# Performance work log

Hardware: AMD Instinct MI355X
Metric: run time of the kernel (lower is better)

Reference implementation:

```python
import jax, jax.numpy as jnp
import numpy as np

WS = 8  # window/grid size, hard-coded in GlobalCirculationBlock
NH = 8  # num_heads


def _ln(x, w, b):
    m = jnp.mean(x, -1, keepdims=True)
    v = jnp.mean((x - m) ** 2, -1, keepdims=True)
    return (x - m) * jax.lax.rsqrt(v + 1e-5) * w + b


def _attn(q, k, v, scale):
    # q,k,v: [..., S, hd]
    s = jnp.einsum('...qd,...kd->...qk', q, k) * scale
    return jnp.einsum('...qk,...kd->...qd', jax.nn.softmax(s, axis=-1), v)


def setup_inputs() -> dict:
    key = jax.random.key(0)
    ks = jax.random.split(key, 8)
    B, C, H, W = 8, 128, 128, 128
    hid = 4 * C
    f = lambda k, shape, s=0.02: jax.random.normal(k, shape, jnp.float32) * s
    z = lambda n: jnp.zeros((n,), jnp.float32)
    return {
        'x': f(ks[0], (B, C, H, W), 1.0),
        'conv_w': f(ks[1], (C, 1, 3, 3)),        # depthwise 3x3 pos embed
        'conv_b': z(C),
        'norm1_w': jnp.ones((C,), jnp.float32), 'norm1_b': z(C),
        'wqkv': f(ks[2], (C, 3 * C)),            # qkv_bias=False
        'proj_w': f(ks[3], (C, C)), 'proj_b': z(C),
        'norm2_w': jnp.ones((C,), jnp.float32), 'norm2_b': z(C),
        'fc1_w': f(ks[4], (C, hid)), 'fc1_b': z(hid),
        'fc2_w': f(ks[5], (hid, C)), 'fc2_b': z(C),
        'ls1': jnp.full((C,), 1e-2, jnp.float32),
        'ls2': jnp.full((C,), 1e-2, jnp.float32),
    }


def reference(x, conv_w, conv_b, norm1_w, norm1_b, wqkv, proj_w, proj_b,
              norm2_w, norm2_b, fc1_w, fc1_b, fc2_w, fc2_b, ls1, ls2):
    B, C, H, W = x.shape
    nh, ws = NH, WS
    hd = C // nh
    scale = hd ** -0.5
    nhl = nh // 2                     # local heads == global heads
    nH, nW = H // ws, W // ws         # H,W multiples of ws -> no padding

    # depthwise conv positional embedding + residual
    pos = jax.lax.conv_general_dilated(
        x, conv_w, (1, 1), 'SAME',
        dimension_numbers=('NCHW', 'OIHW', 'NCHW'), feature_group_count=C)
    x = x + pos + conv_b[None, :, None, None]

    xt = x.reshape(B, C, H * W).transpose(0, 2, 1)   # [B, N, C]

    # ---- dual-scale attention ----
    xn = _ln(xt, norm1_w, norm1_b).reshape(B, H, W, C)
    qkv = (xn @ wqkv).reshape(B, H, W, 3, nh, hd)
    q, k, v = qkv[:, :, :, 0], qkv[:, :, :, 1], qkv[:, :, :, 2]  # [B,H,W,nh,hd]

    # local branch: first nhl heads, window attention (seq = ws*ws)
    def win(t):  # [B,H,W,nhl,hd] -> [B,nH,nW,nhl,ws*ws,hd]
        t = t.reshape(B, nH, ws, nW, ws, nhl, hd)
        return t.transpose(0, 1, 3, 5, 2, 4, 6).reshape(B, nH, nW, nhl, ws * ws, hd)

    ol = _attn(win(q[..., :nhl, :]), win(k[..., :nhl, :]), win(v[..., :nhl, :]), scale)
    ol = (ol.reshape(B, nH, nW, nhl, ws, ws, hd)
            .transpose(0, 1, 4, 2, 5, 3, 6)
            .reshape(B, H, W, nhl * hd))

    # global branch: last nhl heads, grid attention (seq = nH*nW)
    def grd(t):  # [B,H,W,nhl,hd] -> [B,ws,ws,nhl,nH*nW,hd]
        t = t.reshape(B, nH, ws, nW, ws, nhl, hd)
        return t.transpose(0, 2, 4, 5, 1, 3, 6).reshape(B, ws, ws, nhl, nH * nW, hd)

    og = _attn(grd(q[..., nhl:, :]), grd(k[..., nhl:, :]), grd(v[..., nhl:, :]), scale)
    og = (og.reshape(B, ws, ws, nhl, nH, nW, hd)
            .transpose(0, 4, 1, 5, 2, 3, 6)
            .reshape(B, H, W, nhl * hd))

    a = jnp.concatenate([ol, og], axis=-1).reshape(B, H * W, C)
    a = a @ proj_w + proj_b
    xt = xt + ls1 * a

    # ---- MLP ----
    h = _ln(xt, norm2_w, norm2_b)
    h = jax.nn.gelu(h @ fc1_w + fc1_b, approximate=False) @ fc2_w + fc2_b
    xt = xt + ls2 * h

    return xt.transpose(0, 2, 1).reshape(B, C, H, W)
```

## Files before the change

kernel.cpp:

```cpp
#include <hip/hip_runtime.h>
#include <hip/hip_bf16.h>

typedef __hip_bfloat16 bf16;
typedef __attribute__((ext_vector_type(8))) short short8;
typedef __attribute__((ext_vector_type(4))) short short4v;
typedef __attribute__((ext_vector_type(4))) float floatx4;
typedef __attribute__((ext_vector_type(16))) float floatx16;

#define Bn 8
#define Cc 128
#define Hh 128
#define Wl 128
#define HW (Hh*Wl)
#define NT (Bn*HW)
#define REG 8388608

#define QSCALE 0.36067376022224085f
#if __has_builtin(__builtin_amdgcn_exp2f)
#define EXP2(x) __builtin_amdgcn_exp2f(x)
#else
#define EXP2(x) __expf((x)*0.69314718055994531f)
#endif

__device__ __forceinline__ float b2f(bf16 v){ return __bfloat162float(v); }
__device__ __forceinline__ bf16  f2b(float v){ return __float2bfloat16(v); }

#define GL16(gp, lp) __builtin_amdgcn_global_load_lds( \
    (__attribute__((address_space(1))) unsigned int*)(gp), \
    (__attribute__((address_space(3))) unsigned int*)(lp), 16, 0, 0)

__global__ __launch_bounds__(256) void transpose_all(const float* __restrict__ wqkv,
                                                     const float* __restrict__ proj_w,
                                                     const float* __restrict__ fc1_w,
                                                     const float* __restrict__ fc2_w,
                                                     bf16* __restrict__ qkvT,
                                                     bf16* __restrict__ projT,
                                                     bf16* __restrict__ fc1T,
                                                     bf16* __restrict__ fc2T){
  int idx = blockIdx.x*256 + threadIdx.x;
  const float* src; bf16* dst; int K, N;
  if(idx < 49152){ src=wqkv; dst=qkvT; K=128; N=384; }
  else if(idx < 65536){ idx -= 49152; src=proj_w; dst=projT; K=128; N=128; }
  else if(idx < 131072){ idx -= 65536; src=fc1_w; dst=fc1T; K=128; N=512; }
  else { idx -= 131072; src=fc2_w; dst=fc2T; K=512; N=128; }
  int n = idx % N, k = idx / N;
  dst[(size_t)n*K + k] = f2b(src[idx]);
}

__global__ __launch_bounds__(256) void conv_kernel(const float* __restrict__ x,
                                                   const float* __restrict__ cw,
                                                   const float* __restrict__ cb,
                                                   float* __restrict__ xt){
  __shared__ float tile[16][132];
  int blk = blockIdx.x;
  int h = blk & 127; int t = blk >> 7;
  int cg = t & 7;    int b = t >> 3;
  int w4 = threadIdx.x & 31;
  int ci = threadIdx.x >> 5;
  int w0 = w4*4;
#pragma unroll
  for(int cc=0; cc<2; cc++){
    int c = cg*16 + ci*2 + cc;
    const float* xp = x + ((size_t)(b*Cc + c))*HW;
    float wg[9];
#pragma unroll
    for(int i=0;i<9;i++) wg[i] = cw[c*9+i];
    float4 rowv[3]; float lf[3], rt[3];
#pragma unroll
    for(int r=0;r<3;r++){
      int hh = h-1+r;
      float4 v = {0.f,0.f,0.f,0.f};
      if(hh>=0 && hh<Hh) v = *(const float4*)(xp + hh*Wl + w0);
      rowv[r] = v;
      float l = __shfl_up(v.w, 1, 32);
      float rr = __shfl_down(v.x, 1, 32);
      lf[r] = (w4==0)  ? 0.f : l;
      rt[r] = (w4==31) ? 0.f : rr;
    }
    float acc0 = cb[c], acc1 = cb[c], acc2 = cb[c], acc3 = cb[c];
#pragma unroll
    for(int r=0;r<3;r++){
      float4 v = rowv[r];
      acc0 += wg[r*3+0]*lf[r] + wg[r*3+1]*v.x + wg[r*3+2]*v.y;
      acc1 += wg[r*3+0]*v.x   + wg[r*3+1]*v.y + wg[r*3+2]*v.z;
      acc2 += wg[r*3+0]*v.y   + wg[r*3+1]*v.z + wg[r*3+2]*v.w;
      acc3 += wg[r*3+0]*v.z   + wg[r*3+1]*v.w + wg[r*3+2]*rt[r];
    }
    acc0 += rowv[1].x; acc1 += rowv[1].y; acc2 += rowv[1].z; acc3 += rowv[1].w;
    float4 o = {acc0, acc1, acc2, acc3};
    *(float4*)&tile[ci*2+cc][w0] = o;
  }
  __syncthreads();
  const size_t obase = ((size_t)b*HW + (size_t)h*Wl)*Cc + cg*16;
#pragma unroll
  for(int i=0;i<8;i++){
    int idx = i*256 + threadIdx.x;
    int c2 = idx & 15, w2 = idx >> 4;
    xt[obase + (size_t)w2*Cc + c2] = tile[c2][w2];
  }
}

__global__ __launch_bounds__(256) void ln_kernel(const float* __restrict__ xt,
                                                 const float* __restrict__ wv,
                                                 const float* __restrict__ bv,
                                                 bf16* __restrict__ xn){
  int tok  = blockIdx.x*4 + (threadIdx.x>>6);
  int lane = threadIdx.x & 63;
  const float* row = xt + (size_t)tok*Cc;
  float v0 = row[lane], v1 = row[lane+64];
  float s = v0+v1;
#pragma unroll
  for(int off=32; off; off>>=1) s += __shfl_down(s, off, 64);
  s = __shfl(s, 0, 64);
  float m = s * (1.0f/128.0f);
  float d0 = v0-m, d1 = v1-m;
  float vs = d0*d0 + d1*d1;
#pragma unroll
  for(int off=32; off; off>>=1) vs += __shfl_down(vs, off, 64);
  vs = __shfl(vs, 0, 64);
  float rstd = rsqrtf(vs*(1.0f/128.0f) + 1e-5f);
  bf16* orow = xn + (size_t)tok*Cc;
  orow[lane]    = f2b(d0*rstd*wv[lane]    + bv[lane]);
  orow[lane+64] = f2b(d1*rstd*wv[lane+64] + bv[lane+64]);
}

template<int EPI>
__global__ __launch_bounds__(256) void mfma_gemm(const bf16* __restrict__ A,
                                                 const bf16* __restrict__ Wt,
                                                 const float* __restrict__ bias,
                                                 bf16* __restrict__ outb,
                                                 float* __restrict__ xt,
                                                 const float* __restrict__ ls,
                                                 int N, int K){
  __shared__ short As[2][128*32];
  __shared__ short Bs[2][64*32];
  const int tid  = threadIdx.x;
  const int lane = tid & 63;
  const int w    = tid >> 6;

  const int nwg = gridDim.x * gridDim.y;
  const int lin = blockIdx.y * gridDim.x + blockIdx.x;
  const int t   = (lin & 7) * (nwg >> 3) + (lin >> 3);
  const int m0  = (t / gridDim.x) * 128;
  const int n0  = (t % gridDim.x) * 64;

  const int l1 = tid + 256;
  const bf16* gA0 = A  + (size_t)(m0 + ((tid>>6)<<4) + (tid&15))*K + (((tid>>4)&3)<<3);
  const bf16* gA1 = A  + (size_t)(m0 + ((l1 >>6)<<4) + (l1 &15))*K + (((l1 >>4)&3)<<3);
  const bf16* gB  = Wt + (size_t)(n0 + ((tid>>6)<<4) + (tid&15))*K + (((tid>>4)&3)<<3);
  const int ldsA0 = w*512;
  const int ldsA1 = 2048 + w*512;
  const int ldsB  = w*512;

  floatx4 acc[4][2];
#pragma unroll
  for(int i=0;i<4;i++)
#pragma unroll
    for(int j=0;j<2;j++) acc[i][j] = (floatx4){0.f,0.f,0.f,0.f};

  const int nk = K >> 5;
  GL16(gA0, &As[0][ldsA0]);
  GL16(gA1, &As[0][ldsA1]);
  GL16(gB , &Bs[0][ldsB ]);
  __syncthreads();

  int cur = 0;
  for(int it=0; it<nk; ++it){
    if(it+1 < nk){
      const int kn = (it+1) << 5;
      GL16(gA0 + kn, &As[cur^1][ldsA0]);
      GL16(gA1 + kn, &As[cur^1][ldsA1]);
      GL16(gB  + kn, &Bs[cur^1][ldsB ]);
    }
    short8 af[4], bfr[2];
#pragma unroll
    for(int mt=0;mt<4;mt++) af[mt] = *(short8*)&As[cur][(((w&1)*4+mt)*64 + lane)*8];
#pragma unroll
    for(int nt=0;nt<2;nt++) bfr[nt] = *(short8*)&Bs[cur][(((w>>1)*2+nt)*64 + lane)*8];
#pragma unroll
    for(int mt=0;mt<4;mt++)
#pragma unroll
      for(int nt=0;nt<2;nt++)
        acc[mt][nt] = __builtin_amdgcn_mfma_f32_16x16x32_bf16(af[mt], bfr[nt], acc[mt][nt], 0, 0, 0);
    __syncthreads();
    cur ^= 1;
  }

#pragma unroll
  for(int mt=0;mt<4;mt++){
#pragma unroll
    for(int nt=0;nt<2;nt++){
#pragma unroll
      for(int r=0;r<4;r++){
        int row = m0 + (w&1)*64 + mt*16 + ((lane>>4))*4 + r;
        int col = n0 + (w>>1)*32 + nt*16 + (lane&15);
        float v = acc[mt][nt][r];
        if(EPI==0){
          int reg = col >> 6;
          int head = (col >> 4) & 3;
          int ch = col & 15;
          int b = row >> 14, h = (row >> 7) & 127, ww = row & 127;
          if(reg < 2) v *= QSCALE;
          size_t didx;
          if(!(reg & 1)){
            int inst = ((b*16 + (h>>3))*16 + (ww>>3))*4 + head;
            int pos = (h&7)*8 + (ww&7);
            didx = ((size_t)inst*64 + pos)*16 + ch;
          } else {
            int inst = ((b*8 + (h&7))*8 + (ww&7))*4 + head;
            int pos = (h>>3)*16 + (ww>>3);
            didx = ((size_t)inst*256 + pos)*16 + ch;
          }
          outb[(size_t)reg*REG + didx] = f2b(v);
        } else if(EPI==2){
          v += bias[col];
          xt[(size_t)row*128 + col] += ls[col]*v;
        }
      }
    }
  }
}

__global__ __launch_bounds__(256) void fused_mlp(const bf16* A,
                                                 const bf16* __restrict__ W1,
                                                 const float* __restrict__ b1,
                                                 const bf16* __restrict__ W2,
                                                 const float* __restrict__ b2,
                                                 const float* __restrict__ xt,
                                                 const float* __restrict__ ls,
                                                 bf16* outb){
  extern __shared__ short lds[];
  const int W1OFF = 0, W2OFF = 8192, HSOFF = 16384;
  const int tid = threadIdx.x, lane = tid & 63, w = tid >> 6;
  const int n16 = lane & 15, quad = lane >> 4;
  const int lin = blockIdx.x;
  const int t = (lin & 7)*128 + (lin >> 3);
  const int mw = t*128 + w*32;

  auto stage = [&](int nc, int buf){
    const bf16* W1c = W1 + (size_t)nc*32*128;
#pragma unroll
    for(int p=0;p<2;p++){
      int fid = p*4 + w;
      int nt = fid >> 2, ks = fid & 3;
      GL16(W1c + (size_t)(nt*16 + n16)*128 + ks*32 + quad*8, &lds[W1OFF + buf*4096 + fid*512]);
      GL16(W2 + (size_t)(fid*16 + n16)*512 + nc*32 + quad*8, &lds[W2OFF + buf*4096 + fid*512]);
    }
  };

  short8 areg[2][4];
#pragma unroll
  for(int mt=0;mt<2;mt++)
#pragma unroll
    for(int ks=0;ks<4;ks++)
      areg[mt][ks] = *(const short8*)(A + (size_t)(mw + mt*16 + n16)*128 + ks*32 + quad*8);

  floatx4 acc2[2][8];
#pragma unroll
  for(int i=0;i<2;i++)
#pragma unroll
    for(int j=0;j<8;j++) acc2[i][j] = (floatx4){0.f,0.f,0.f,0.f};

  short* hw = &lds[HSOFF + w*1280];

  stage(0, 0);
  __syncthreads();

  for(int nc=0; nc<16; ++nc){
    const int cur = nc & 1;
    if(nc+1 < 16) stage(nc+1, cur^1);

    const short* W1b = &lds[W1OFF + cur*4096];
    floatx4 acc1[2][2];
#pragma unroll
    for(int i=0;i<2;i++)
#pragma unroll
      for(int j=0;j<2;j++) acc1[i][j] = (floatx4){0.f,0.f,0.f,0.f};
#pragma unroll
    for(int ks=0;ks<4;ks++){
#pragma unroll
      for(int nt=0;nt<2;nt++){
        short8 bfr = *(const short8*)&W1b[(nt*4+ks)*512 + lane*8];
#pragma unroll
        for(int mt=0;mt<2;mt++)
          acc1[mt][nt] = __builtin_amdgcn_mfma_f32_16x16x32_bf16(areg[mt][ks], bfr, acc1[mt][nt], 0, 0, 0);
      }
    }

#pragma unroll
    for(int nt=0;nt<2;nt++){
      float bb = b1[nc*32 + nt*16 + n16];
#pragma unroll
      for(int mt=0;mt<2;mt++){
#pragma unroll
        for(int r=0;r<4;r++){
          float v = acc1[mt][nt][r] + bb;
          float u = v*v;
          float e = EXP2(v*__fmaf_rn(u, 0.044715f, 1.0f)*(-2.3022127f));
          float g = v*__builtin_amdgcn_rcpf(1.0f + e);
          bf16 gb = f2b(g);
          hw[(mt*16 + quad*4 + r)*40 + nt*16 + n16] = *(short*)&gb;
        }
      }
    }

    const short* W2b = &lds[W2OFF + cur*4096];
    short8 ha[2];
#pragma unroll
    for(int mt=0;mt<2;mt++) ha[mt] = *(short8*)&hw[(mt*16 + n16)*40 + quad*8];
#pragma unroll
    for(int nt2=0;nt2<8;nt2++){
      short8 bf2 = *(const short8*)&W2b[nt2*512 + lane*8];
#pragma unroll
      for(int mt=0;mt<2;mt++)
        acc2[mt][nt2] = __builtin_amdgcn_mfma_f32_16x16x32_bf16(ha[mt], bf2, acc2[mt][nt2], 0, 0, 0);
    }

    __syncthreads();
  }

#pragma unroll
  for(int nt2=0;nt2<8;nt2++){
    int col = nt2*16 + n16;
    float bb = b2[col], lsv = ls[col];
#pragma unroll
    for(int mt=0;mt<2;mt++){
#pragma unroll
      for(int r=0;r<4;r++){
        int row = mw + mt*16 + quad*4 + r;
        float v = acc2[mt][nt2][r] + bb;
        float rr = xt[(size_t)row*128 + col] + lsv*v;
        outb[(size_t)row*128 + col] = f2b(rr);
      }
    }
  }
}

__global__ __launch_bounds__(256) void attn_local2(const bf16* __restrict__ qL,
                                                   const bf16* __restrict__ kL,
                                                   const bf16* __restrict__ vL,
                                                   bf16* __restrict__ a){
  __shared__ short vt[16*72];
  __shared__ short pb[4][16*72];
  const int tid = threadIdx.x;
  const int w = tid >> 6, lane = tid & 63;
  const int n16 = lane & 15, quad = lane >> 4;
  const int blk = blockIdx.x;
  const int head = blk & 3, winid = blk >> 2;
  const bf16* Qb = qL + (size_t)blk*1024;
  const bf16* Kb = kL + (size_t)blk*1024;
  const bf16* Vb = vL + (size_t)blk*1024;

  if(tid < 128){
    int tok = tid >> 1, u = tid & 1;
    short8 v = *(const short8*)(Vb + tok*16 + u*8);
#pragma unroll
    for(int i=0;i<8;i++) vt[(u*8+i)*72 + tok] = ((short*)&v)[i];
  }
  __syncthreads();

  const int qt = w;
  short8 qf = {0,0,0,0,0,0,0,0};
  if(quad < 2) qf = *(const short8*)(Qb + (qt*16+n16)*16 + quad*8);

  floatx4 sf[4];
#pragma unroll
  for(int kt=0; kt<4; kt++){
    short8 kf = {0,0,0,0,0,0,0,0};
    if(quad < 2) kf = *(const short8*)(Kb + (kt*16+n16)*16 + quad*8);
    floatx4 z = (floatx4){0.f,0.f,0.f,0.f};
    sf[kt] = __builtin_amdgcn_mfma_f32_16x16x32_bf16(qf, kf, z, 0, 0, 0);
  }

  float mx[4] = {-1e30f,-1e30f,-1e30f,-1e30f};
#pragma unroll
  for(int kt=0; kt<4; kt++)
#pragma unroll
    for(int r=0;r<4;r++) mx[r] = fmaxf(mx[r], sf[kt][r]);
#pragma unroll
  for(int r=0;r<4;r++){
    mx[r] = fmaxf(mx[r], __shfl_xor(mx[r], 1, 64));
    mx[r] = fmaxf(mx[r], __shfl_xor(mx[r], 2, 64));
    mx[r] = fmaxf(mx[r], __shfl_xor(mx[r], 4, 64));
    mx[r] = fmaxf(mx[r], __shfl_xor(mx[r], 8, 64));
    mx[r] = -mx[r];
  }
  float l[4] = {0.f,0.f,0.f,0.f};
#pragma unroll
  for(int kt=0; kt<4; kt++){
#pragma unroll
    for(int r=0;r<4;r++){
      float p = EXP2(sf[kt][r] + mx[r]);
      l[r] += p;
      bf16 pbv = f2b(p);
      pb[w][(quad*4+r)*72 + kt*16 + n16] = *(short*)&pbv;
    }
  }
#pragma unroll
  for(int r=0;r<4;r++){
    l[r] += __shfl_xor(l[r], 1, 64);
    l[r] += __shfl_xor(l[r], 2, 64);
    l[r] += __shfl_xor(l[r], 4, 64);
    l[r] += __shfl_xor(l[r], 8, 64);
  }

  floatx4 of = (floatx4){0.f,0.f,0.f,0.f};
#pragma unroll
  for(int kb=0; kb<2; kb++){
    short8 pf = *(short8*)&pb[w][n16*72 + kb*32 + quad*8];
    short8 vfb = *(short8*)&vt[n16*72 + kb*32 + quad*8];
    of = __builtin_amdgcn_mfma_f32_16x16x32_bf16(pf, vfb, of, 0, 0, 0);
  }

  const int wj = winid & 15, wi = (winid >> 4) & 15, b = winid >> 8;
  const int ooff = head*16;
#pragma unroll
  for(int r=0;r<4;r++){
    int pos = qt*16 + quad*4 + r;
    int h = wi*8 + (pos>>3), ww = wj*8 + (pos&7);
    size_t t = (size_t)b*HW + (size_t)h*Wl + ww;
    a[t*Cc + ooff + n16] = f2b(of[r] / l[r]);
  }
}

__global__ __launch_bounds__(256) void attn_grid2(const bf16* __restrict__ qG,
                                                  const bf16* __restrict__ kG,
                                                  const bf16* __restrict__ vG,
                                                  bf16* __restrict__ a){
  __shared__ short vt[16*264];
  __shared__ short pb[4][32*136];
  const int tid = threadIdx.x;
  const int w = tid >> 6, lane = tid & 63;
  const int n16 = lane & 15, quad = lane >> 4;
  const int q32 = lane & 31, hb = lane >> 5;
  const int blk = blockIdx.x;
  const int head = blk & 3, ginst = blk >> 2;
  const bf16* Qb = qG + (size_t)blk*4096;
  const bf16* Kb = kG + (size_t)blk*4096;
  const bf16* Vb = vG + (size_t)blk*4096;

#pragma unroll
  for(int it=0; it<2; it++){
    int chunk = it*256 + tid;
    int tok = chunk >> 1, u = chunk & 1;
    short8 v = *(const short8*)(Vb + tok*16 + u*8);
#pragma unroll
    for(int i=0;i<8;i++) vt[(u*8+i)*264 + tok] = ((short*)&v)[i];
  }
  __syncthreads();

  const int sj = ginst & 7, si = (ginst >> 3) & 7, b = ginst >> 6;
  const int ooff = 64 + head*16;
  short* pbw = pb[w];
  const floatx16 Z16 = {0.f,0.f,0.f,0.f,0.f,0.f,0.f,0.f,0.f,0.f,0.f,0.f,0.f,0.f,0.f,0.f};

#pragma unroll
  for(int qi=0; qi<2; qi++){
    const int q0 = w*64 + qi*32;
    const short8 qf = *(const short8*)(Qb + (size_t)(q0 + q32)*16 + hb*8);
    float l_acc = 0.f;
    floatx4 of0 = (floatx4){0.f,0.f,0.f,0.f};
    floatx4 of1 = (floatx4){0.f,0.f,0.f,0.f};
#pragma unroll
    for(int kc=0; kc<2; kc++){
#pragma unroll
      for(int kt=0; kt<4; kt++){
        short8 kf = *(const short8*)(Kb + (size_t)(kc*128 + kt*32 + q32)*16 + hb*8);
        floatx16 s = __builtin_amdgcn_mfma_f32_32x32x16_bf16(kf, qf, Z16, 0, 0, 0);
#pragma unroll
        for(int g=0; g<4; g++){
          float p0 = EXP2(s[4*g+0]);
          float p1 = EXP2(s[4*g+1]);
          float p2 = EXP2(s[4*g+2]);
          float p3 = EXP2(s[4*g+3]);
          l_acc += (p0+p1)+(p2+p3);
          short4v pk = { (short)__bfloat16_as_ushort(f2b(p0)),
                         (short)__bfloat16_as_ushort(f2b(p1)),
                         (short)__bfloat16_as_ushort(f2b(p2)),
                         (short)__bfloat16_as_ushort(f2b(p3)) };
          *(short4v*)&pbw[q32*136 + kt*32 + g*8 + hb*4] = pk;
        }
      }
#pragma unroll
      for(int kb=0; kb<4; kb++){
        short8 vf  = *(short8*)&vt[n16*264 + kc*128 + kb*32 + quad*8];
        short8 pf0 = *(short8*)&pbw[n16*136 + kb*32 + quad*8];
        of0 = __builtin_amdgcn_mfma_f32_16x16x32_bf16(pf0, vf, of0, 0, 0, 0);
        short8 pf1 = *(short8*)&pbw[(16+n16)*136 + kb*32 + quad*8];
        of1 = __builtin_amdgcn_mfma_f32_16x16x32_bf16(pf1, vf, of1, 0, 0, 0);
      }
    }
    l_acc += __shfl_xor(l_acc, 32, 64);
#pragma unroll
    for(int hf=0; hf<2; hf++){
      floatx4 of = hf ? of1 : of0;
#pragma unroll
      for(int r=0;r<4;r++){
        float lr = __shfl(l_acc, hf*16 + quad*4 + r, 64);
        int pos = q0 + hf*16 + quad*4 + r;
        int h = (pos>>4)*8 + si, ww = (pos&15)*8 + sj;
        size_t t = (size_t)b*HW + (size_t)h*Wl + ww;
        a[t*Cc + ooff + n16] = f2b(of[r] / lr);
      }
    }
  }
}

__global__ __launch_bounds__(256) void transpose_kernel(const bf16* __restrict__ xf,
                                                        float* __restrict__ out){
  __shared__ bf16 tile[32][33];
  int t0 = blockIdx.x*32, c0 = blockIdx.y*32, b = blockIdx.z;
  int x = threadIdx.x, y = threadIdx.y;
  const bf16* src = xf + (size_t)b*HW*Cc;
  float* dst = out + (size_t)b*Cc*HW;
#pragma unroll
  for(int i=0;i<4;i++)
    tile[y*4+i][x] = src[(size_t)(t0 + y*4+i)*Cc + c0 + x];
  __syncthreads();
#pragma unroll
  for(int i=0;i<4;i++)
    dst[(size_t)(c0 + y*4+i)*HW + t0 + x] = b2f(tile[x][y*4+i]);
}

extern "C" void kernel_launch(void* const* d_in, const int* in_sizes, int n_in,
                              void* d_out, int out_size, void* d_ws, size_t ws_size,
                              hipStream_t stream) {
  const float* x       = (const float*)d_in[0];
  const float* conv_w  = (const float*)d_in[1];
  const float* conv_b  = (const float*)d_in[2];
  const float* norm1_w = (const float*)d_in[3];
  const float* norm1_b = (const float*)d_in[4];
  const float* wqkv    = (const float*)d_in[5];
  const float* proj_w  = (const float*)d_in[6];
  const float* proj_b  = (const float*)d_in[7];
  const float* norm2_w = (const float*)d_in[8];
  const float* norm2_b = (const float*)d_in[9];
  const float* fc1_w   = (const float*)d_in[10];
  const float* fc1_b   = (const float*)d_in[11];
  const float* fc2_w   = (const float*)d_in[12];
  const float* fc2_b   = (const float*)d_in[13];
  const float* ls1     = (const float*)d_in[14];
  const float* ls2     = (const float*)d_in[15];
  float* out = (float*)d_out;

  char* ws = (char*)d_ws;
  float* xt = (float*)ws;
  bf16*  sh = (bf16*)(ws + (size_t)NT*Cc*4);
  bf16*  qh = (bf16*)(ws + (size_t)NT*Cc*4 + (size_t)NT*Cc*2);
  bf16*  wt = (bf16*)(ws + (size_t)NT*Cc*4 + (size_t)NT*Cc*2 + (size_t)NT*512*2);
  bf16* qkvT = wt;
  bf16* projT= wt + 49152;
  bf16* fc1T = wt + 65536;
  bf16* fc2T = wt + 131072;

  transpose_all<<<196608/256, 256, 0, stream>>>(wqkv, proj_w, fc1_w, fc2_w,
                                                qkvT, projT, fc1T, fc2T);
  conv_kernel<<<Bn*8*Hh, 256, 0, stream>>>(x, conv_w, conv_b, xt);
  ln_kernel<<<NT/4, 256, 0, stream>>>(xt, norm1_w, norm1_b, sh);
  mfma_gemm<0><<<dim3(384/64, NT/128), 256, 0, stream>>>(sh, qkvT, nullptr, qh, nullptr, nullptr, 384, 128);
  attn_grid2<<<2048, 256, 0, stream>>>(qh + (size_t)1*REG, qh + (size_t)3*REG, qh + (size_t)5*REG, sh);
  attn_local2<<<8192, 256, 0, stream>>>(qh + (size_t)0*REG, qh + (size_t)2*REG, qh + (size_t)4*REG, sh);
  mfma_gemm<2><<<dim3(128/64, NT/128), 256, 0, stream>>>(sh, projT, proj_b, nullptr, xt, ls1, 128, 128);
  ln_kernel<<<NT/4, 256, 0, stream>>>(xt, norm2_w, norm2_b, sh);
  fused_mlp<<<NT/128, 256, 43008, stream>>>(sh, fc1T, fc1_b, fc2T, fc2_b, xt, ls2, sh);
  transpose_kernel<<<dim3(HW/32, Cc/32, Bn), dim3(32,8), 0, stream>>>(sh, out);
}
```

Before: 442.7 us.

## Fuse LayerNorm2 and output transpose into fused MLP kernel

Computes the second LayerNorm inside the fused MLP kernel, reading fp32 xt directly instead of a separate ln_kernel writing bf16. The epilogue stages results through LDS and writes fp32 NCHW output directly, removing the separate transpose kernel and the bf16 round trip. This drops two launches and several full-tensor memory passes, at the cost of extra syncs in the epilogue and a single-pass variance formula.

```diff
diff --git a/kernel.cpp b/kernel.cpp
--- a/kernel.cpp
+++ b/kernel.cpp
@@ -221,14 +221,15 @@
   }
 }
 
-__global__ __launch_bounds__(256) void fused_mlp(const bf16* A,
+__global__ __launch_bounds__(256) void fused_mlp(const float* __restrict__ xt,
                                                  const bf16* __restrict__ W1,
                                                  const float* __restrict__ b1,
                                                  const bf16* __restrict__ W2,
                                                  const float* __restrict__ b2,
-                                                 const float* __restrict__ xt,
+                                                 const float* __restrict__ nw,
+                                                 const float* __restrict__ nb,
                                                  const float* __restrict__ ls,
-                                                 bf16* outb){
+                                                 float* __restrict__ out){
   extern __shared__ short lds[];
   const int W1OFF = 0, W2OFF = 8192, HSOFF = 16384;
   const int tid = threadIdx.x, lane = tid & 63, w = tid >> 6;
@@ -248,12 +249,43 @@
     }
   };
 
+  stage(0, 0);
+
+  float wreg[4][8], breg[4][8];
+#pragma unroll
+  for(int ks=0;ks<4;ks++){
+    *(float4*)&wreg[ks][0] = *(const float4*)(nw + ks*32 + quad*8);
+    *(float4*)&wreg[ks][4] = *(const float4*)(nw + ks*32 + quad*8 + 4);
+    *(float4*)&breg[ks][0] = *(const float4*)(nb + ks*32 + quad*8);
+    *(float4*)&breg[ks][4] = *(const float4*)(nb + ks*32 + quad*8 + 4);
+  }
   short8 areg[2][4];
 #pragma unroll
-  for(int mt=0;mt<2;mt++)
-#pragma unroll
-    for(int ks=0;ks<4;ks++)
-      areg[mt][ks] = *(const short8*)(A + (size_t)(mw + mt*16 + n16)*128 + ks*32 + quad*8);
+  for(int mt=0;mt<2;mt++){
+    const float* xr = xt + (size_t)(mw + mt*16 + n16)*128;
+    float av[4][8]; float s = 0.f, qs = 0.f;
+#pragma unroll
+    for(int ks=0;ks<4;ks++){
+      *(float4*)&av[ks][0] = *(const float4*)(xr + ks*32 + quad*8);
+      *(float4*)&av[ks][4] = *(const float4*)(xr + ks*32 + quad*8 + 4);
+#pragma unroll
+      for(int j=0;j<8;j++){ s += av[ks][j]; qs += av[ks][j]*av[ks][j]; }
+    }
+    s  += __shfl_xor(s, 16, 64);  s  += __shfl_xor(s, 32, 64);
+    qs += __shfl_xor(qs, 16, 64); qs += __shfl_xor(qs, 32, 64);
+    float m = s*(1.0f/128.0f);
+    float rstd = rsqrtf(qs*(1.0f/128.0f) - m*m + 1e-5f);
+#pragma unroll
+    for(int ks=0;ks<4;ks++){
+      short8 t8;
+#pragma unroll
+      for(int j=0;j<8;j++){
+        bf16 g = f2b((av[ks][j]-m)*rstd*wreg[ks][j] + breg[ks][j]);
+        ((short*)&t8)[j] = *(short*)&g;
+      }
+      areg[mt][ks] = t8;
+    }
+  }
 
   floatx4 acc2[2][8];
 #pragma unroll
@@ -263,7 +295,6 @@
 
   short* hw = &lds[HSOFF + w*1280];
 
-  stage(0, 0);
   __syncthreads();
 
   for(int nc=0; nc<16; ++nc){
@@ -319,6 +350,12 @@
     __syncthreads();
   }
 
+  const int t128 = t*128;
+  const int bI = t128 >> 14;
+  const int hw0 = t128 & (HW-1);
+  float* op = out + (size_t)bI*Cc*HW + hw0;
+  float* tlf = (float*)lds;
+  const int cI = tid >> 4, toff = (tid & 15)*8;
 #pragma unroll
   for(int nt2=0;nt2<8;nt2++){
     int col = nt2*16 + n16;
@@ -329,10 +366,15 @@
       for(int r=0;r<4;r++){
         int row = mw + mt*16 + quad*4 + r;
         float v = acc2[mt][nt2][r] + bb;
-        float rr = xt[(size_t)row*128 + col] + lsv*v;
-        outb[(size_t)row*128 + col] = f2b(rr);
-      }
-    }
+        tlf[n16*132 + (w*32 + mt*16 + quad*4 + r)] = xt[(size_t)row*128 + col] + lsv*v;
+      }
+    }
+    __syncthreads();
+    float4 v0 = *(float4*)&tlf[cI*132 + toff];
+    float4 v1 = *(float4*)&tlf[cI*132 + toff + 4];
+    *(float4*)&op[(size_t)(nt2*16 + cI)*HW + toff]     = v0;
+    *(float4*)&op[(size_t)(nt2*16 + cI)*HW + toff + 4] = v1;
+    __syncthreads();
   }
 }
 
@@ -504,22 +546,6 @@
       }
     }
   }
-}
-
-__global__ __launch_bounds__(256) void transpose_kernel(const bf16* __restrict__ xf,
-                                                        float* __restrict__ out){
-  __shared__ bf16 tile[32][33];
-  int t0 = blockIdx.x*32, c0 = blockIdx.y*32, b = blockIdx.z;
-  int x = threadIdx.x, y = threadIdx.y;
-  const bf16* src = xf + (size_t)b*HW*Cc;
-  float* dst = out + (size_t)b*Cc*HW;
-#pragma unroll
-  for(int i=0;i<4;i++)
-    tile[y*4+i][x] = src[(size_t)(t0 + y*4+i)*Cc + c0 + x];
-  __syncthreads();
-#pragma unroll
-  for(int i=0;i<4;i++)
-    dst[(size_t)(c0 + y*4+i)*HW + t0 + x] = b2f(tile[x][y*4+i]);
 }
 
 extern "C" void kernel_launch(void* const* d_in, const int* in_sizes, int n_in,
@@ -561,7 +587,6 @@
   attn_grid2<<<2048, 256, 0, stream>>>(qh + (size_t)1*REG, qh + (size_t)3*REG, qh + (size_t)5*REG, sh);
   attn_local2<<<8192, 256, 0, stream>>>(qh + (size_t)0*REG, qh + (size_t)2*REG, qh + (size_t)4*REG, sh);
   mfma_gemm<2><<<dim3(128/64, NT/128), 256, 0, stream>>>(sh, projT, proj_b, nullptr, xt, ls1, 128, 128);
-  ln_kernel<<<NT/4, 256, 0, stream>>>(xt, norm2_w, norm2_b, sh);
-  fused_mlp<<<NT/128, 256, 43008, stream>>>(sh, fc1T, fc1_b, fc2T, fc2_b, xt, ls2, sh);
-  transpose_kernel<<<dim3(HW/32, Cc/32, Bn), dim3(32,8), 0, stream>>>(sh, out);
-}
+  fused_mlp<<<NT/128, 256, 43008, stream>>>(xt, fc1T, fc1_b, fc2T, fc2_b,
+                                            norm2_w, norm2_b, ls2, out);
+}
```

Measured after the change: 401.7 us. 1.1x faster.
